# Optimization experiments

Hardware: AMD Instinct MI355X
Metric: run time of the kernel (lower is better)

The kernel has to match this reference:

```python
import jax, jax.numpy as jnp
import numpy as np

B, S, D, H, M, V, R = 2, 1024, 768, 8, 3072, 32000, 2
HD = D // H  # head_dim = qkv_dim // num_heads


def ln(x, scale, bias, eps=1e-6):
    m = jnp.mean(x, axis=-1, keepdims=True)
    v = jnp.mean(jnp.square(x - m), axis=-1, keepdims=True)
    return (x - m) * jax.lax.rsqrt(v + eps) * scale + bias


def setup_inputs() -> dict:
    key = jax.random.key(0)
    ks = jax.random.split(key, 16)
    r = lambda i, shp, s=0.02: jax.random.normal(ks[i], shp, jnp.float32) * s
    z = lambda shp: jnp.zeros(shp, jnp.float32)
    o = lambda shp: jnp.ones(shp, jnp.float32)
    return {
        'l2r_embed': jax.random.normal(ks[0], (B, S, D), jnp.float32),
        'r2l_embed': jax.random.normal(ks[1], (B, S, D), jnp.float32),
        'temb': jax.random.normal(ks[2], (B, D), jnp.float32),
        'ln_l2r_s': o((D,)), 'ln_l2r_b': z((D,)),
        'ln_r2l_s': o((D,)), 'ln_r2l_b': z((D,)),
        'Wq': r(3, (D, H, HD)), 'bq': z((H, HD)),
        'Wk': r(4, (D, H, HD)), 'bk': z((H, HD)),
        'Wv': r(5, (D, H, HD)), 'bv': z((H, HD)),
        'Wo': r(6, (H, HD, D)), 'bo': z((D,)),
        'ff_ln_s': o((D,)), 'ff_ln_b': z((D,)),
        'ff_w1': r(7, (D, M)), 'ff_b1': z((M,)),
        'ff_w2': r(8, (M, D)), 'ff_b2': z((D,)),
        'tm_w1': r(9, (D, M)), 'tm_b1': z((M,)),
        'tm_w2': r(10, (M, 4 * D)), 'tm_b2': z((4 * D,)),
        'film_w': r(11, (R, 4 * D, 2 * D)), 'film_b': z((R, 2 * D)),
        'r_w1': r(12, (R, D, M)), 'r_b1': z((R, M)),
        'r_w2': r(13, (R, M, D)), 'r_b2': z((R, D)),
        'r_ln_s': o((R, D)), 'r_ln_b': z((R, D)),
        'out_w': r(14, (D, V)), 'out_b': z((V,)),
    }


def reference(l2r_embed, r2l_embed, temb, ln_l2r_s, ln_l2r_b, ln_r2l_s, ln_r2l_b,
              Wq, bq, Wk, bk, Wv, bv, Wo, bo, ff_ln_s, ff_ln_b,
              ff_w1, ff_b1, ff_w2, ff_b2, tm_w1, tm_b1, tm_w2, tm_b2,
              film_w, film_b, r_w1, r_b1, r_w2, r_b2, r_ln_s, r_ln_b,
              out_w, out_b):
    inputs = l2r_embed + r2l_embed
    # prenorm on each direction (temb stays raw)
    l2r_n = ln(l2r_embed, ln_l2r_s, ln_l2r_b)
    r2l_n = ln(r2l_embed, ln_r2l_s, ln_r2l_b)
    # cross attention: query from sum, keys/vals from [temb, l2r, r2l]
    q = jnp.einsum('bsd,dhk->bshk', l2r_n + r2l_n, Wq) + bq
    all_e = jnp.concatenate([temb[:, None, :], l2r_n, r2l_n], axis=1)  # [B, 2S+1, D]
    k = jnp.einsum('bsd,dhk->bshk', all_e, Wk) + bk
    v = jnp.einsum('bsd,dhk->bshk', all_e, Wv) + bv
    q = q / jnp.sqrt(jnp.float32(HD))
    logits = jnp.einsum('bqhd,bkhd->bhqk', q, k)  # [B, H, S, 2S+1]
    idx = jnp.arange(S)
    l2r_mask = idx[:, None] >= idx[None, :]
    r2l_mask = idx[:, None] <= idx[None, :]
    joint = jnp.concatenate(
        [jnp.ones((S, 1), bool), l2r_mask, r2l_mask], axis=-1)[None, None]
    aw = jax.nn.softmax(
        jnp.where(joint, logits, jnp.finfo(jnp.float32).min), axis=-1)
    x = jnp.einsum('bhqk,bkhd->bqhd', aw, v)
    x = jnp.einsum('bqhd,hde->bqe', x, Wo) + bo
    x = x + inputs
    # prenorm FF block
    z = ln(x, ff_ln_s, ff_ln_b)
    z = jax.nn.relu(z @ ff_w1 + ff_b1) @ ff_w2 + ff_b2
    x = x + z
    # residual readout with FiLM conditioning
    t = jax.nn.gelu(temb @ tm_w1 + tm_b1) @ tm_w2 + tm_b2  # [B, 4D]
    for i in range(R):
        film = t @ film_w[i] + film_b[i]  # [B, 2D]
        z = jax.nn.gelu(x @ r_w1[i] + r_b1[i]) @ r_w2[i] + r_b2[i]
        x = ln(x + z, r_ln_s[i], r_ln_b[i])
        a, b = jnp.split(film[:, None, :], 2, axis=-1)
        x = a * x + b
    return x @ out_w + out_b  # [B, S, V]
```

## Files before the change

### kernel.cpp

```cpp
#include <hip/hip_runtime.h>
#include <cstdint>
#include <cstddef>

#define Bb 2
#define Ss 1024
#define Dd 768
#define Hh 8
#define HDh 96
#define Mm 3072
#define Vv 32000
#define KVr 2049

typedef __attribute__((ext_vector_type(8))) short short8v;
typedef __attribute__((ext_vector_type(4))) short short4v;
typedef __attribute__((ext_vector_type(4))) float f32x4;

#define GL16(gp, lp) __builtin_amdgcn_global_load_lds( \
    (const __attribute__((address_space(1))) void*)(gp), \
    (__attribute__((address_space(3))) void*)(lp), 16, 0, 0)

static __device__ __forceinline__ short f2bf(float f) {
  union { float f; unsigned u; } x; x.f = f;
  unsigned r = (x.u + 0x7FFFu + ((x.u >> 16) & 1u)) >> 16;
  return (short)(r & 0xFFFFu);
}

static __device__ __forceinline__ float gelu_f(float v) {
  float u = 0.7978845608028654f * (v + 0.044715f * v * v * v);
  float au = fabsf(u);
  float e = __expf(2.f * au);
  float t = 1.f - 2.f / (e + 1.f);
  return 0.5f * v * (1.f + copysignf(t, u));
}

static __device__ __forceinline__ float blk_sum(float val, float* sh) {
  #pragma unroll
  for (int off = 32; off >= 1; off >>= 1) val += __shfl_xor(val, off);
  __syncthreads();
  if ((threadIdx.x & 63) == 0) sh[threadIdx.x >> 6] = val;
  __syncthreads();
  return sh[0] + sh[1] + sh[2] + sh[3];
}

__global__ __launch_bounds__(256) void prep_kernel(
    const float* __restrict__ l2r, const float* __restrict__ r2l,
    const float* __restrict__ temb,
    const float* __restrict__ s1, const float* __restrict__ b1,
    const float* __restrict__ s2, const float* __restrict__ b2,
    float* __restrict__ inputs, short* __restrict__ qin, short* __restrict__ all_e)
{
  __shared__ float sh[4];
  const int tid = threadIdx.x;
  if (blockIdx.x >= 2048) {
    int b = blockIdx.x - 2048;
    #pragma unroll
    for (int i = 0; i < 3; ++i)
      all_e[(size_t)b * KVr * Dd + tid + i * 256] = f2bf(temb[(size_t)b * Dd + tid + i * 256]);
    return;
  }
  const int row = blockIdx.x;
  const int b = row >> 10, s = row & 1023;
  const float* ap = l2r + (size_t)row * Dd;
  const float* cp = r2l + (size_t)row * Dd;
  float a0 = ap[tid], a1 = ap[tid + 256], a2 = ap[tid + 512];
  float c0 = cp[tid], c1 = cp[tid + 256], c2 = cp[tid + 512];
  float ma = blk_sum(a0 + a1 + a2, sh) * (1.f / 768.f);
  float mc = blk_sum(c0 + c1 + c2, sh) * (1.f / 768.f);
  float va = blk_sum((a0-ma)*(a0-ma) + (a1-ma)*(a1-ma) + (a2-ma)*(a2-ma), sh) * (1.f / 768.f);
  float vc = blk_sum((c0-mc)*(c0-mc) + (c1-mc)*(c1-mc) + (c2-mc)*(c2-mc), sh) * (1.f / 768.f);
  float ia = rsqrtf(va + 1e-6f), ic = rsqrtf(vc + 1e-6f);
  size_t ro = (size_t)row * Dd;
  size_t e1 = ((size_t)b * KVr + 1 + s) * Dd;
  size_t e2 = ((size_t)b * KVr + 1 + Ss + s) * Dd;
  float av[3] = {a0, a1, a2}, cv[3] = {c0, c1, c2};
  #pragma unroll
  for (int i = 0; i < 3; ++i) {
    int c = tid + i * 256;
    float an = (av[i] - ma) * ia * s1[c] + b1[c];
    float cn = (cv[i] - mc) * ic * s2[c] + b2[c];
    inputs[ro + c] = av[i] + cv[i];
    qin[ro + c]    = f2bf(an + cn);
    all_e[e1 + c]  = f2bf(an);
    all_e[e2 + c]  = f2bf(cn);
  }
}

__global__ __launch_bounds__(256) void ln_comb2(
    const float* __restrict__ pk,
    const float* __restrict__ bias, const float* __restrict__ res,
    const float* __restrict__ sc, const float* __restrict__ bi,
    float* __restrict__ yf, short* __restrict__ yb)
{
  __shared__ float sh[4];
  const int row = blockIdx.x, tid = threadIdx.x;
  const size_t PS = (size_t)2048 * 768;
  size_t ro = (size_t)row * Dd;
  float vv[3];
  #pragma unroll
  for (int i = 0; i < 3; ++i) {
    int c = tid + i * 256;
    vv[i] = pk[ro + c] + pk[PS + ro + c] + bias[c] + res[ro + c];
  }
  float m = blk_sum(vv[0] + vv[1] + vv[2], sh) * (1.f / 768.f);
  float var = blk_sum((vv[0]-m)*(vv[0]-m) + (vv[1]-m)*(vv[1]-m) + (vv[2]-m)*(vv[2]-m), sh) * (1.f / 768.f);
  float inv = rsqrtf(var + 1e-6f);
  #pragma unroll
  for (int i = 0; i < 3; ++i) {
    int c = tid + i * 256;
    yf[ro + c] = vv[i];
    yb[ro + c] = f2bf((vv[i] - m) * inv * sc[c] + bi[c]);
  }
}

__global__ __launch_bounds__(256) void scale_comb(
    const float* __restrict__ pk, const float* __restrict__ bias,
    short* __restrict__ yb, float scale)
{
  const int row = blockIdx.x, tid = threadIdx.x;
  const size_t PS = (size_t)2048 * 768;
  size_t ro = (size_t)row * Dd;
  #pragma unroll
  for (int i = 0; i < 3; ++i) {
    int c = tid + i * 256;
    yb[ro + c] = f2bf((pk[ro + c] + pk[PS + ro + c] + bias[c]) * scale);
  }
}

__global__ __launch_bounds__(256) void ln_comb(
    const float* __restrict__ pk,
    const float* __restrict__ bias, const float* __restrict__ res,
    const float* __restrict__ sc, const float* __restrict__ bi,
    const float* __restrict__ film, float* __restrict__ yf, short* __restrict__ yb)
{
  __shared__ float sh[4];
  const int row = blockIdx.x, tid = threadIdx.x;
  const size_t PS = (size_t)2048 * 768;
  size_t ro = (size_t)row * Dd;
  float vv[3];
  #pragma unroll
  for (int i = 0; i < 3; ++i) {
    int c = tid + i * 256;
    float v = bias[c] + res[ro + c];
    #pragma unroll
    for (int s = 0; s < 4; ++s) v += pk[s * PS + ro + c];
    vv[i] = v;
  }
  float m = blk_sum(vv[0] + vv[1] + vv[2], sh) * (1.f / 768.f);
  float var = blk_sum((vv[0]-m)*(vv[0]-m) + (vv[1]-m)*(vv[1]-m) + (vv[2]-m)*(vv[2]-m), sh) * (1.f / 768.f);
  float inv = rsqrtf(var + 1e-6f);
  int bb = row >> 10;
  #pragma unroll
  for (int i = 0; i < 3; ++i) {
    int c = tid + i * 256;
    float o = (vv[i] - m) * inv * sc[c] + bi[c];
    o = film[(size_t)bb * 1536 + c] * o + film[(size_t)bb * 1536 + 768 + c];
    if (yf) yf[ro + c] = o;
    if (yb) yb[ro + c] = f2bf(o);
  }
}

__global__ __launch_bounds__(256) void combine_kernel(
    const float* __restrict__ pk,
    const float* __restrict__ bias, const float* __restrict__ res,
    float* __restrict__ yf, short* __restrict__ yb)
{
  const int row = blockIdx.x, tid = threadIdx.x;
  const size_t PS = (size_t)2048 * 768;
  size_t ro = (size_t)row * Dd;
  #pragma unroll
  for (int i = 0; i < 3; ++i) {
    int c = tid + i * 256;
    float v = bias[c] + res[ro + c];
    #pragma unroll
    for (int s = 0; s < 4; ++s) v += pk[s * PS + ro + c];
    yf[ro + c] = v;
    yb[ro + c] = f2bf(v);
  }
}

__global__ __launch_bounds__(256) void convT(const float* __restrict__ W, short* __restrict__ Wt,
                                             int K, int N, int ntile)
{
  __shared__ short T[64][72];
  const int bn = blockIdx.x % ntile, bk = blockIdx.x / ntile;
  const int k0 = bk * 64, n0 = bn * 64, tid = threadIdx.x;
  #pragma unroll
  for (int i = 0; i < 4; ++i) {
    int id = i * 256 + tid;
    int r = id >> 4, c4 = (id & 15) * 4;
    float4 w4 = *(const float4*)(W + (size_t)(k0 + r) * N + n0 + c4);
    T[c4 + 0][r] = f2bf(w4.x);
    T[c4 + 1][r] = f2bf(w4.y);
    T[c4 + 2][r] = f2bf(w4.z);
    T[c4 + 3][r] = f2bf(w4.w);
  }
  __syncthreads();
  #pragma unroll
  for (int i = 0; i < 4; ++i) {
    int id = i * 256 + tid;
    int n = id >> 4, k4 = (id & 15) * 4;
    short4v s = *(const short4v*)&T[n][k4];
    *(short4v*)(Wt + (size_t)(n0 + n) * K + k0 + k4) = s;
  }
}

__global__ __launch_bounds__(256) void convT2(const float* __restrict__ W1, short* __restrict__ D1,
                                              const float* __restrict__ W2, short* __restrict__ D2)
{
  __shared__ short T[64][72];
  const int tid = threadIdx.x;
  const bool second = blockIdx.x >= 576;
  const int id576 = second ? (blockIdx.x - 576) : blockIdx.x;
  const int K = second ? 3072 : 768;
  const int N = second ? 768 : 3072;
  const int ntile = N >> 6;
  const float* W = second ? W2 : W1;
  short* Wt = second ? D2 : D1;
  const int bn = id576 % ntile, bk = id576 / ntile;
  const int k0 = bk * 64, n0 = bn * 64;
  #pragma unroll
  for (int i = 0; i < 4; ++i) {
    int id = i * 256 + tid;
    int r = id >> 4, c4 = (id & 15) * 4;
    float4 w4 = *(const float4*)(W + (size_t)(k0 + r) * N + n0 + c4);
    T[c4 + 0][r] = f2bf(w4.x);
    T[c4 + 1][r] = f2bf(w4.y);
    T[c4 + 2][r] = f2bf(w4.z);
    T[c4 + 3][r] = f2bf(w4.w);
  }
  __syncthreads();
  #pragma unroll
  for (int i = 0; i < 4; ++i) {
    int id = i * 256 + tid;
    int n = id >> 4, k4 = (id & 15) * 4;
    short4v s = *(const short4v*)&T[n][k4];
    *(short4v*)(Wt + (size_t)(n0 + n) * K + k0 + k4) = s;
  }
}

__global__ __launch_bounds__(256) void convT4(const float* __restrict__ W0, const float* __restrict__ W1,
                                              const float* __restrict__ W2, const float* __restrict__ W3,
                                              const float* __restrict__ bk, const float* __restrict__ bv,
                                              short* __restrict__ Wt, float* __restrict__ kvb,
                                              const float* __restrict__ part2c, const float* __restrict__ fb,
                                              float* __restrict__ f0, float* __restrict__ f1)
{
  __shared__ short T[64][72];
  const int tid = threadIdx.x;
  if (blockIdx.x >= 577) {
    const int n = (blockIdx.x - 577) * 256 + tid;
    float a0 = fb[n], a1 = a0;
    for (int s = 0; s < 64; ++s) {
      a0 += part2c[(size_t)s * 6144 + n];
      a1 += part2c[(size_t)s * 6144 + 3072 + n];
    }
    float* dst = (n < 1536) ? f0 : f1;
    const int c = (n >= 1536) ? (n - 1536) : n;
    dst[c] = a0;
    dst[1536 + c] = a1;
    return;
  }
  if (blockIdx.x == 576) {
    #pragma unroll
    for (int i = 0; i < 6; ++i) {
      int c = i * 256 + tid;
      if (c < 1536) kvb[c] = (c < 768) ? bk[c] : bv[c - 768];
    }
    return;
  }
  const int wsel = blockIdx.x / 144, rem = blockIdx.x % 144;
  const float* W = wsel == 0 ? W0 : wsel == 1 ? W1 : wsel == 2 ? W2 : W3;
  short* dst = Wt + (size_t)wsel * 768 * 768;
  const int bn = rem % 12, bk2 = rem / 12;
  const int k0 = bk2 * 64, n0 = bn * 64;
  #pragma unroll
  for (int i = 0; i < 4; ++i) {
    int id = i * 256 + tid;
    int r = id >> 4, c4 = (id & 15) * 4;
    float4 w4 = *(const float4*)(W + (size_t)(k0 + r) * 768 + n0 + c4);
    T[c4 + 0][r] = f2bf(w4.x);
    T[c4 + 1][r] = f2bf(w4.y);
    T[c4 + 2][r] = f2bf(w4.z);
    T[c4 + 3][r] = f2bf(w4.w);
  }
  __syncthreads();
  #pragma unroll
  for (int i = 0; i < 4; ++i) {
    int id = i * 256 + tid;
    int n = id >> 4, k4 = (id & 15) * 4;
    short4v s = *(const short4v*)&T[n][k4];
    *(short4v*)(dst + (size_t)(n0 + n) * 768 + k0 + k4) = s;
  }
}

template<int ACT>
__global__ __launch_bounds__(256, 4) void gemm_bf(
    const short* __restrict__ A, const short* __restrict__ Bt,
    const float* __restrict__ bias, const float* __restrict__ res,
    float* __restrict__ C, short* __restrict__ Cbf, float* __restrict__ Cpart,
    int M, int N, int K, float scale, int mtiles, int ntiles, int ksplit)
{
  __shared__ short As[2][4096];
  __shared__ short Bs[2][4096];
  const int tid = threadIdx.x, lane = tid & 63, wv = tid >> 6;
  const int l15 = lane & 15, l4 = lane >> 4;

  const int nwg = gridDim.x;
  const int qc = nwg >> 3, rc = nwg & 7;
  const int xcd = blockIdx.x & 7, idx = blockIdx.x >> 3;
  const int wgid = (xcd < rc ? xcd * (qc + 1) : rc * (qc + 1) + (xcd - rc) * qc) + idx;
  const int by = wgid % mtiles;
  const int rest = wgid / mtiles;
  const int bx = rest % ntiles;
  const int sp = rest / ntiles;
  const int kper = K / ksplit;
  const int kbeg = sp * kper;
  const int NT = kper >> 5;

  const int m0 = by * 128, n0 = bx * 128;
  const int wm = (wv >> 1) * 64, wn = (wv & 1) * 64;

  const int srow = lane >> 2, schunk = lane & 3;
  const int scsw = (schunk ^ ((srow >> 1) & 3)) << 3;
  const short* sA = A + (size_t)(m0 + wv * 32 + srow) * K + kbeg + scsw;
  const short* sB = Bt + (size_t)(n0 + wv * 32 + srow) * K + kbeg + scsw;
  const int stBase = wv * 1024;
  const int frsw = (l4 ^ ((l15 >> 1) & 3)) << 3;

  f32x4 acc[4][4];
  const f32x4 zz = {0.f, 0.f, 0.f, 0.f};
  #pragma unroll
  for (int i = 0; i < 4; ++i)
    #pragma unroll
    for (int j = 0; j < 4; ++j) acc[i][j] = zz;

  GL16(sA, &As[0][stBase]);
  GL16(sA + (size_t)16 * K, &As[0][stBase + 512]);
  GL16(sB, &Bs[0][stBase]);
  GL16(sB + (size_t)16 * K, &Bs[0][stBase + 512]);

  int buf = 0;
  for (int t = 0; t < NT; ++t) {
    if (t + 1 < NT) {
      int k0 = (t + 1) << 5;
      GL16(sA + k0, &As[buf ^ 1][stBase]);
      GL16(sA + (size_t)16 * K + k0, &As[buf ^ 1][stBase + 512]);
      GL16(sB + k0, &Bs[buf ^ 1][stBase]);
      GL16(sB + (size_t)16 * K + k0, &Bs[buf ^ 1][stBase + 512]);
      asm volatile("s_waitcnt vmcnt(4)" ::: "memory");
    } else {
      asm volatile("s_waitcnt vmcnt(0)" ::: "memory");
    }
    __builtin_amdgcn_s_barrier();

    short8v af[4], bfv[4];
    #pragma unroll
    for (int mi = 0; mi < 4; ++mi)
      af[mi] = *(const short8v*)&As[buf][(wm + mi * 16 + l15) * 32 + frsw];
    #pragma unroll
    for (int ni = 0; ni < 4; ++ni)
      bfv[ni] = *(const short8v*)&Bs[buf][(wn + ni * 16 + l15) * 32 + frsw];
    __builtin_amdgcn_s_setprio(1);
    #pragma unroll
    for (int mi = 0; mi < 4; ++mi)
      #pragma unroll
      for (int ni = 0; ni < 4; ++ni)
        acc[mi][ni] = __builtin_amdgcn_mfma_f32_16x16x32_bf16(af[mi], bfv[ni], acc[mi][ni], 0, 0, 0);
    __builtin_amdgcn_s_setprio(0);
    if (t + 1 < NT) __builtin_amdgcn_s_barrier();
    buf ^= 1;
  }

  if (Cpart) {
    float* Cp = Cpart + (size_t)sp * M * N;
    #pragma unroll
    for (int mi = 0; mi < 4; ++mi)
      #pragma unroll
      for (int r = 0; r < 4; ++r) {
        int row = m0 + wm + mi * 16 + l4 * 4 + r;
        if (row >= M) continue;
        size_t rb = (size_t)row * N;
        #pragma unroll
        for (int ni = 0; ni < 4; ++ni)
          Cp[rb + n0 + wn + ni * 16 + l15] = acc[mi][ni][r];
      }
    return;
  }

  #pragma unroll
  for (int mi = 0; mi < 4; ++mi) {
    #pragma unroll
    for (int r = 0; r < 4; ++r) {
      int row = m0 + wm + mi * 16 + l4 * 4 + r;
      if (row >= M) continue;
      size_t rb = (size_t)row * N;
      #pragma unroll
      for (int ni = 0; ni < 4; ++ni) {
        int col = n0 + wn + ni * 16 + l15;
        float val = (acc[mi][ni][r] + bias[col]) * scale;
        if (ACT == 1) val = fmaxf(val, 0.f);
        if (ACT == 2) val = gelu_f(val);
        if (res) val += res[rb + col];
        if (C)   C[rb + col] = val;
        if (Cbf) Cbf[rb + col] = f2bf(val);
      }
    }
  }
}

__global__ __launch_bounds__(512, 2) void gemm256(
    const short* __restrict__ A, const short* __restrict__ Bt,
    const float* __restrict__ bias, float* __restrict__ C,
    int M, int N, int K, int mtiles)
{
  __shared__ short As[2][16384];
  __shared__ short Bs[2][16384];
  const int tid = threadIdx.x, lane = tid & 63, wv = tid >> 6;
  const int l15 = lane & 15, l4 = lane >> 4;

  const int nwg = gridDim.x;
  const int qc = nwg >> 3, rc = nwg & 7;
  const int xcd = blockIdx.x & 7, idx = blockIdx.x >> 3;
  const int wgid = (xcd < rc ? xcd * (qc + 1) : rc * (qc + 1) + (xcd - rc) * qc) + idx;
  const int by = wgid % mtiles, bx = wgid / mtiles;
  const int m0 = by * 256, n0 = bx * 256;
  const int wm = (wv >> 2) * 128, wn = (wv & 3) * 64;

  const int srow = lane >> 2, schunk = lane & 3;
  const int scsw = (schunk ^ ((srow >> 1) & 3)) << 3;
  const short* sA = A + (size_t)(m0 + wv * 16 + srow) * K + scsw;
  const short* sB = Bt + (size_t)(n0 + wv * 16 + srow) * K + scsw;
  const int stBase = wv * 512;
  const int frsw = (l4 ^ ((l15 >> 1) & 3)) << 3;

  #define STG_A(b, kk, ko) do { \
    GL16(sA + (ko) + (kk) * 32,                  &As[b][(kk) * 8192 + stBase]); \
    GL16(sA + (size_t)128 * K + (ko) + (kk) * 32, &As[b][(kk) * 8192 + 4096 + stBase]); } while (0)
  #define STG_B(b, kk, ko) do { \
    GL16(sB + (ko) + (kk) * 32,                  &Bs[b][(kk) * 8192 + stBase]); \
    GL16(sB + (size_t)128 * K + (ko) + (kk) * 32, &Bs[b][(kk) * 8192 + 4096 + stBase]); } while (0)
  #define ARD(b, kk, row) (*(const short8v*)&As[b][(kk) * 8192 + (row) * 32 + frsw])
  #define BRD(b, kk, row) (*(const short8v*)&Bs[b][(kk) * 8192 + (row) * 32 + frsw])

  f32x4 acc[8][4];
  const f32x4 zz = {0.f, 0.f, 0.f, 0.f};
  #pragma unroll
  for (int i = 0; i < 8; ++i)
    #pragma unroll
    for (int j = 0; j < 4; ++j) acc[i][j] = zz;

  const int NT = K >> 6;

  STG_A(0, 0, 0); STG_B(0, 0, 0); STG_A(0, 1, 0); STG_B(0, 1, 0);
  asm volatile("s_waitcnt vmcnt(4)" ::: "memory");
  __builtin_amdgcn_s_barrier();

  int buf = 0;
  for (int t = 0; t < NT; ++t) {
    const bool pf = (t + 1 < NT);
    const int k1 = (t + 1) << 6;
    short8v af[4], bfv[4];

    #pragma unroll
    for (int mi = 0; mi < 4; ++mi) af[mi] = ARD(buf, 0, wm + mi * 16 + l15);
    #pragma unroll
    for (int ni = 0; ni < 4; ++ni) bfv[ni] = BRD(buf, 0, wn + ni * 16 + l15);
    if (pf) STG_A(buf ^ 1, 0, k1);
    __builtin_amdgcn_s_barrier();
    asm volatile("s_waitcnt lgkmcnt(0)" ::: "memory");
    __builtin_amdgcn_sched_barrier(0);
    __builtin_amdgcn_s_setprio(1);
    #pragma unroll
    for (int mi = 0; mi < 4; ++mi)
      #pragma unroll
      for (int ni = 0; ni < 4; ++ni)
        acc[mi][ni] = __builtin_amdgcn_mfma_f32_16x16x32_bf16(af[mi], bfv[ni], acc[mi][ni], 0, 0, 0);
    __builtin_amdgcn_s_setprio(0);
    __builtin_amdgcn_s_barrier();

    #pragma unroll
    for (int mi = 0; mi < 4; ++mi) af[mi] = ARD(buf, 0, wm + 64 + mi * 16 + l15);
    if (pf) STG_B(buf ^ 1, 0, k1);
    __builtin_amdgcn_s_barrier();
    asm volatile("s_waitcnt lgkmcnt(0)" ::: "memory");
    __builtin_amdgcn_sched_barrier(0);
    __builtin_amdgcn_s_setprio(1);
    #pragma unroll
    for (int mi = 0; mi < 4; ++mi)
      #pragma unroll
      for (int ni = 0; ni < 4; ++ni)
        acc[4 + mi][ni] = __builtin_amdgcn_mfma_f32_16x16x32_bf16(af[mi], bfv[ni], acc[4 + mi][ni], 0, 0, 0);
    __builtin_amdgcn_s_setprio(0);
    if (pf) asm volatile("s_waitcnt vmcnt(4)" ::: "memory");
    else    asm volatile("s_waitcnt vmcnt(0)" ::: "memory");
    __builtin_amdgcn_s_barrier();

    #pragma unroll
    for (int mi = 0; mi < 4; ++mi) af[mi] = ARD(buf, 1, wm + mi * 16 + l15);
    #pragma unroll
    for (int ni = 0; ni < 4; ++ni) bfv[ni] = BRD(buf, 1, wn + ni * 16 + l15);
    if (pf) STG_A(buf ^ 1, 1, k1);
    __builtin_amdgcn_s_barrier();
    asm volatile("s_waitcnt lgkmcnt(0)" ::: "memory");
    __builtin_amdgcn_sched_barrier(0);
    __builtin_amdgcn_s_setprio(1);
    #pragma unroll
    for (int mi = 0; mi < 4; ++mi)
      #pragma unroll
      for (int ni = 0; ni < 4; ++ni)
        acc[mi][ni] = __builtin_amdgcn_mfma_f32_16x16x32_bf16(af[mi], bfv[ni], acc[mi][ni], 0, 0, 0);
    __builtin_amdgcn_s_setprio(0);
    __builtin_amdgcn_s_barrier();

    #pragma unroll
    for (int mi = 0; mi < 4; ++mi) af[mi] = ARD(buf, 1, wm + 64 + mi * 16 + l15);
    if (pf) STG_B(buf ^ 1, 1, k1);
    __builtin_amdgcn_s_barrier();
    asm volatile("s_waitcnt lgkmcnt(0)" ::: "memory");
    __builtin_amdgcn_sched_barrier(0);
    __builtin_amdgcn_s_setprio(1);
    #pragma unroll
    for (int mi = 0; mi < 4; ++mi)
      #pragma unroll
      for (int ni = 0; ni < 4; ++ni)
        acc[4 + mi][ni] = __builtin_amdgcn_mfma_f32_16x16x32_bf16(af[mi], bfv[ni], acc[4 + mi][ni], 0, 0, 0);
    __builtin_amdgcn_s_setprio(0);
    if (pf) asm volatile("s_waitcnt vmcnt(4)" ::: "memory");
    __builtin_amdgcn_s_barrier();

    buf ^= 1;
  }

  #pragma unroll
  for (int mi = 0; mi < 8; ++mi) {
    #pragma unroll
    for (int r = 0; r < 4; ++r) {
      int row = m0 + wm + mi * 16 + l4 * 4 + r;
      size_t rb = (size_t)row * N;
      #pragma unroll
      for (int ni = 0; ni < 4; ++ni) {
        int col = n0 + wn + ni * 16 + l15;
        C[rb + col] = acc[mi][ni][r] + bias[col];
      }
    }
  }
  #undef STG_A
  #undef STG_B
  #undef ARD
  #undef BRD
}

__global__ __launch_bounds__(256) void attn_kernel(
    const short* __restrict__ q, const short* __restrict__ kv,
    float* __restrict__ Op0, float* __restrict__ Op1, float* __restrict__ ml)
{
  __shared__ short Kls[64][104];
  __shared__ short Vt[96][72];
  __shared__ short Pls[4][16][72];

  const int tid = threadIdx.x, lane = tid & 63, w = tid >> 6;
  const int l15 = lane & 15, l4 = lane >> 4;
  const int chunk = blockIdx.x >> 8;
  const int inner = blockIdx.x & 255;
  const int qt = inner & 15;
  const int bh = inner >> 4;
  const int h = bh & 7, b = bh >> 3;
  const int qb = qt * 64;
  const int qw = qb + w * 16;

  short8v qf[3];
  {
    const short* qp = q + ((size_t)(b * Ss + qw + l15)) * Dd + h * HDh + l4 * 8;
    #pragma unroll
    for (int kk = 0; kk < 3; ++kk) qf[kk] = *(const short8v*)(qp + kk * 32);
  }

  const f32x4 zz = {0.f, 0.f, 0.f, 0.f};
  f32x4 Oa[6];
  #pragma unroll
  for (int fn = 0; fn < 6; ++fn) Oa[fn] = zz;
  float mrow[4], lrow[4];
  #pragma unroll
  for (int r = 0; r < 4; ++r) { mrow[r] = -3.0e38f; lrow[r] = 0.f; }

  const size_t kvbase = (size_t)b * KVr;

  for (int t = chunk; t < 33; t += 2) {
    int k0 = t * 64;
    bool l2r_vis = (k0 <= Ss) && (k0 - 1 <= qb + 63);
    int rmaxk = (k0 + 63 > 2 * Ss) ? 2 * Ss : (k0 + 63);
    bool r2l_vis = (k0 + 63 >= Ss + 1) && (rmaxk - (Ss + 1) >= qb);
    if (!(t == 0 || l2r_vis || r2l_vis)) continue;

    __syncthreads();
    #pragma unroll
    for (int i = 0; i < 3; ++i) {
      int id = i * 256 + tid;
      int row = id / 12, cc = (id % 12) * 8;
      const short* kp = kv + (kvbase + k0 + row) * 1536 + h * HDh + cc;
      short8v k8 = *(const short8v*)kp;
      *(short8v*)&Kls[row][cc] = k8;
      short8v v8 = *(const short8v*)(kp + 768);
      #pragma unroll
      for (int j = 0; j < 8; ++j) Vt[cc + j][row] = v8[j];
    }
    __syncthreads();

    f32x4 sc[4];
    #pragma unroll
    for (int nt = 0; nt < 4; ++nt) {
      f32x4 d = zz;
      #pragma unroll
      for (int kk = 0; kk < 3; ++kk) {
        short8v kf = *(const short8v*)&Kls[nt * 16 + l15][kk * 32 + l4 * 8];
        d = __builtin_amdgcn_mfma_f32_16x16x32_bf16(qf[kk], kf, d, 0, 0, 0);
      }
      sc[nt] = d;
    }
    float tmax[4] = {-3.0e38f, -3.0e38f, -3.0e38f, -3.0e38f};
    #pragma unroll
    for (int nt = 0; nt < 4; ++nt)
      #pragma unroll
      for (int r = 0; r < 4; ++r) {
        int qg = qw + l4 * 4 + r;
        int j = k0 + nt * 16 + l15;
        bool vis = (j == 0) ||
                   (j >= 1 && j <= Ss && (j - 1) <= qg) ||
                   (j >= Ss + 1 && j <= 2 * Ss && (j - (Ss + 1)) >= qg);
        if (!vis) sc[nt][r] = -3.0e38f;
        tmax[r] = fmaxf(tmax[r], sc[nt][r]);
      }
    #pragma unroll
    for (int r = 0; r < 4; ++r) {
      #pragma unroll
      for (int off = 8; off >= 1; off >>= 1) tmax[r] = fmaxf(tmax[r], __shfl_xor(tmax[r], off));
    }
    float scl[4];
    #pragma unroll
    for (int r = 0; r < 4; ++r) {
      float mnew = fmaxf(mrow[r], tmax[r]);
      scl[r] = __expf(mrow[r] - mnew);
      mrow[r] = mnew;
    }
    #pragma unroll
    for (int fn = 0; fn < 6; ++fn)
      #pragma unroll
      for (int r = 0; r < 4; ++r) Oa[fn][r] *= scl[r];
    float lad[4] = {0.f, 0.f, 0.f, 0.f};
    #pragma unroll
    for (int nt = 0; nt < 4; ++nt)
      #pragma unroll
      for (int r = 0; r < 4; ++r) {
        float p = __expf(sc[nt][r] - mrow[r]);
        lad[r] += p;
        Pls[w][l4 * 4 + r][nt * 16 + l15] = f2bf(p);
      }
    #pragma unroll
    for (int r = 0; r < 4; ++r) {
      #pragma unroll
      for (int off = 8; off >= 1; off >>= 1) lad[r] += __shfl_xor(lad[r], off);
      lrow[r] = lrow[r] * scl[r] + lad[r];
    }
    __syncthreads();

    short8v pf[2];
    #pragma unroll
    for (int kk = 0; kk < 2; ++kk) pf[kk] = *(const short8v*)&Pls[w][l15][kk * 32 + l4 * 8];
    #pragma unroll
    for (int fn = 0; fn < 6; ++fn) {
      #pragma unroll
      for (int kk = 0; kk < 2; ++kk) {
        short8v vf = *(const short8v*)&Vt[fn * 16 + l15][kk * 32 + l4 * 8];
        Oa[fn] = __builtin_amdgcn_mfma_f32_16x16x32_bf16(pf[kk], vf, Oa[fn], 0, 0, 0);
      }
    }
  }

  float* Op = chunk ? Op1 : Op0;
  #pragma unroll
  for (int fn = 0; fn < 6; ++fn)
    #pragma unroll
    for (int r = 0; r < 4; ++r) {
      int row = qw + l4 * 4 + r;
      int col = h * HDh + fn * 16 + l15;
      Op[((size_t)(b * Ss + row)) * Dd + col] = Oa[fn][r];
    }
  if (l15 == 0) {
    #pragma unroll
    for (int r = 0; r < 4; ++r) {
      int row = qw + l4 * 4 + r;
      size_t ix = ((size_t)((chunk * 2 + b) * 8 + h) * 1024 + row) * 2;
      ml[ix] = mrow[r];
      ml[ix + 1] = lrow[r];
    }
  }
}

__global__ __launch_bounds__(256) void attn_merge(
    const float* __restrict__ Op0, const float* __restrict__ Op1,
    const float* __restrict__ ml, short* __restrict__ o)
{
  const int row = blockIdx.x, tid = threadIdx.x;
  const int b = row >> 10, s = row & 1023;
  size_t ro = (size_t)row * Dd;
  #pragma unroll
  for (int i = 0; i < 3; ++i) {
    int c = tid + i * 256;
    int h = c / HDh;
    size_t ix = ((size_t)(b * 8 + h) * 1024 + s) * 2;
    float m0 = ml[ix],         l0 = ml[ix + 1];
    float m1 = ml[32768 + ix], l1 = ml[32768 + ix + 1];
    float mm = fmaxf(m0, m1);
    float s0 = __expf(m0 - mm), s1 = __expf(m1 - mm);
    float denom = s0 * l0 + s1 * l1;
    o[ro + c] = f2bf((s0 * Op0[ro + c] + s1 * Op1[ro + c]) / denom);
  }
}

__global__ __launch_bounds__(256) void thin1(const float* __restrict__ A, const float* __restrict__ W,
                                             float* __restrict__ part, int K, int N, int nblk, int splits)
{
  __shared__ float a0s[64], a1s[64];
  const int nb = blockIdx.x % nblk, ks = blockIdx.x / nblk;
  const int kl = K / splits, kbeg = ks * kl;
  const int tid = threadIdx.x;
  for (int k = tid; k < kl; k += 256) { a0s[k] = A[kbeg + k]; a1s[k] = A[K + kbeg + k]; }
  __syncthreads();
  const int n = nb * 256 + tid;
  float acc0 = 0.f, acc1 = 0.f;
  for (int k = 0; k < kl; ++k) {
    float w = W[(size_t)(kbeg + k) * N + n];
    acc0 = fmaf(a0s[k], w, acc0);
    acc1 = fmaf(a1s[k], w, acc1);
  }
  part[(size_t)ks * 2 * N + n] = acc0;
  part[(size_t)ks * 2 * N + N + n] = acc1;
}

__global__ __launch_bounds__(256) void thin1p(
    const float* __restrict__ pin, const float* __restrict__ bin,
    const float* __restrict__ W, float* __restrict__ part)
{
  __shared__ float a0s[48], a1s[48];
  const int nb = blockIdx.x % 12, ks = blockIdx.x / 12;
  const int kbeg = ks * 48, tid = threadIdx.x;
  for (int j = tid; j < 96; j += 256) {
    int row = j / 48, k = j % 48;
    float v = bin[kbeg + k];
    for (int s = 0; s < 64; ++s) v += pin[(size_t)s * 6144 + (size_t)row * 3072 + kbeg + k];
    v = gelu_f(v);
    if (row) a1s[k] = v; else a0s[k] = v;
  }
  __syncthreads();
  const int n = nb * 256 + tid;
  float acc0 = 0.f, acc1 = 0.f;
  for (int k = 0; k < 48; ++k) {
    float w = W[(size_t)(kbeg + k) * 3072 + n];
    acc0 = fmaf(a0s[k], w, acc0);
    acc1 = fmaf(a1s[k], w, acc1);
  }
  part[(size_t)ks * 6144 + n] = acc0;
  part[(size_t)ks * 6144 + 3072 + n] = acc1;
}

__global__ __launch_bounds__(256) void film1p(
    const float* __restrict__ pin, const float* __restrict__ bin,
    const float* __restrict__ W, float* __restrict__ part)
{
  __shared__ float a0s[48], a1s[48];
  const int nb = blockIdx.x % 12, ks = blockIdx.x / 12;
  const int kbeg = ks * 48, tid = threadIdx.x;
  for (int j = tid; j < 96; j += 256) {
    int row = j / 48, k = j % 48;
    float v = bin[kbeg + k];
    for (int s = 0; s < 64; ++s) v += pin[(size_t)s * 6144 + (size_t)row * 3072 + kbeg + k];
    if (row) a1s[k] = v; else a0s[k] = v;
  }
  __syncthreads();
  const int n = nb * 256 + tid;
  const int col = (n >= 1536) ? (n - 1536) : n;
  const float* Wp = W + ((n < 1536) ? (size_t)0 : (size_t)3072 * 1536)
                      + (size_t)kbeg * 1536 + col;
  float acc0 = 0.f, acc1 = 0.f;
  for (int k = 0; k < 48; ++k) {
    float w = Wp[(size_t)k * 1536];
    acc0 = fmaf(a0s[k], w, acc0);
    acc1 = fmaf(a1s[k], w, acc1);
  }
  part[(size_t)ks * 6144 + n] = acc0;
  part[(size_t)ks * 6144 + 3072 + n] = acc1;
}

static void gemm_launch(int act, const short* A, const short* Bt, const float* bias,
                        const float* res, float* C, short* Cbf, float* Cpart,
                        int M, int N, int K, float scale, int ksplit, hipStream_t s)
{
  int mt = (M + 127) >> 7, nt = N >> 7;
  dim3 grid(mt * nt * ksplit), blk(256);
  if (act == 1)      gemm_bf<1><<<grid, blk, 0, s>>>(A, Bt, bias, res, C, Cbf, Cpart, M, N, K, scale, mt, nt, ksplit);
  else if (act == 2) gemm_bf<2><<<grid, blk, 0, s>>>(A, Bt, bias, res, C, Cbf, Cpart, M, N, K, scale, mt, nt, ksplit);
  else               gemm_bf<0><<<grid, blk, 0, s>>>(A, Bt, bias, res, C, Cbf, Cpart, M, N, K, scale, mt, nt, ksplit);
}

static void conv_launch(const float* W, short* Wt, int K, int N, hipStream_t s)
{
  int nt = N >> 6, kt = K >> 6;
  convT<<<dim3(nt * kt), dim3(256), 0, s>>>(W, Wt, K, N, nt);
}

extern "C" void kernel_launch(void* const* d_in, const int* in_sizes, int n_in,
                              void* d_out, int out_size, void* d_ws, size_t ws_size,
                              hipStream_t stream)
{
  (void)in_sizes; (void)n_in; (void)out_size; (void)ws_size;
  const float* l2r      = (const float*)d_in[0];
  const float* r2l      = (const float*)d_in[1];
  const float* temb     = (const float*)d_in[2];
  const float* ln_l2r_s = (const float*)d_in[3];
  const float* ln_l2r_b = (const float*)d_in[4];
  const float* ln_r2l_s = (const float*)d_in[5];
  const float* ln_r2l_b = (const float*)d_in[6];
  const float* Wq = (const float*)d_in[7];
  const float* bq = (const float*)d_in[8];
  const float* Wk = (const float*)d_in[9];
  const float* bk = (const float*)d_in[10];
  const float* Wv = (const float*)d_in[11];
  const float* bv = (const float*)d_in[12];
  const float* Wo = (const float*)d_in[13];
  const float* bo = (const float*)d_in[14];
  const float* ff_ln_s = (const float*)d_in[15];
  const float* ff_ln_b = (const float*)d_in[16];
  const float* ff_w1 = (const float*)d_in[17];
  const float* ff_b1 = (const float*)d_in[18];
  const float* ff_w2 = (const float*)d_in[19];
  const float* ff_b2 = (const float*)d_in[20];
  const float* tm_w1 = (const float*)d_in[21];
  const float* tm_b1 = (const float*)d_in[22];
  const float* tm_w2 = (const float*)d_in[23];
  const float* tm_b2 = (const float*)d_in[24];
  const float* film_w = (const float*)d_in[25];
  const float* film_b = (const float*)d_in[26];
  const float* r_w1 = (const float*)d_in[27];
  const float* r_b1 = (const float*)d_in[28];
  const float* r_w2 = (const float*)d_in[29];
  const float* r_b2 = (const float*)d_in[30];
  const float* r_ln_s = (const float*)d_in[31];
  const float* r_ln_b = (const float*)d_in[32];
  const float* out_w = (const float*)d_in[33];
  const float* out_b = (const float*)d_in[34];

  uint8_t* base = (uint8_t*)d_ws;
  short* qin_bf  = (short*)(base + 0);
  short* alle_bf = (short*)(base + 3145728);
  short* qb      = (short*)(base + 9440256);
  short* kvbuf   = (short*)(base + 12585984);
  short* attn_bf = (short*)(base + 25175040);
  float* inputs  = (float*)(base + 28320768);
  float* xbuf    = (float*)(base + 34612224);
  short* xn_bf   = (short*)(base + 40903680);
  short* big_bf  = (short*)(base + 44049408);
  float* x2f     = (float*)(base + 56632320);
  short* x2bf    = (short*)(base + 62923776);
  float* x3f     = (float*)(base + 72360960);
  short* x3bf    = (short*)(base + 78652416);
  short* x4bf    = (short*)(base + 81798144);
  short* wslot   = (short*)(base + 84943872);
  uint8_t* sm    = base + 89662464;
  float* f0    = (float*)(sm + 0);
  float* f1    = (float*)(sm + 12288);
  float* kvbia = (float*)(sm + 24576);
  short* w2slot = (short*)inputs;
  float* part2a = (float*)(base + 44049408);
  float* part2b = (float*)(base + 44049408 + 1572864);
  float* part2c = (float*)(base + 44049408 + 3145728);
  float* qpart = (float*)(base + 56632320);
  float* Op0 = (float*)(base + 0);
  float* mlb = (float*)(base + 6291456);
  float* Op1 = xbuf;
  float* wopart = (float*)(base + 0);
  float* partK = (float*)(base + 0);
  short* outwT = (short*)(base + 0);

  const float qscale = 0.1020620726159658f;
  dim3 blk(256);

  thin1<<<dim3(12 * 64), blk, 0, stream>>>(temb, tm_w1, part2a, 768, 3072, 12, 64);
  thin1p<<<dim3(12 * 64), blk, 0, stream>>>(part2a, tm_b1, tm_w2, part2b);
  film1p<<<dim3(12 * 64), blk, 0, stream>>>(part2b, tm_b2, film_w, part2c);

  prep_kernel<<<2050, blk, 0, stream>>>(l2r, r2l, temb, ln_l2r_s, ln_l2r_b, ln_r2l_s, ln_r2l_b,
                                        inputs, qin_bf, alle_bf);

  convT4<<<dim3(589), blk, 0, stream>>>(Wq, Wk, Wv, Wo, bk, bv, wslot, kvbia,
                                        part2c, film_b, f0, f1);

  gemm_launch(0, qin_bf, wslot, bq, nullptr, nullptr, nullptr, qpart, 2048, 768, 768, 1.f, 2, stream);
  scale_comb<<<2048, blk, 0, stream>>>(qpart, bq, qb, qscale);
  gemm_launch(0, alle_bf, wslot + (size_t)768 * 768, kvbia, nullptr, nullptr, kvbuf, nullptr, 4098, 1536, 768, 1.f, 1, stream);

  attn_kernel<<<512, blk, 0, stream>>>(qb, kvbuf, Op0, Op1, mlb);
  attn_merge<<<2048, blk, 0, stream>>>(Op0, Op1, mlb, attn_bf);

  gemm_launch(0, attn_bf, wslot + (size_t)3 * 768 * 768, bo, nullptr, nullptr, nullptr, wopart, 2048, 768, 768, 1.f, 2, stream);
  ln_comb2<<<2048, blk, 0, stream>>>(wopart, bo, inputs, ff_ln_s, ff_ln_b, xbuf, xn_bf);

  convT2<<<dim3(1152), blk, 0, stream>>>(ff_w1, wslot, ff_w2, w2slot);
  gemm_launch(1, xn_bf, wslot, ff_b1, nullptr, nullptr, big_bf, nullptr, 2048, 3072, 768, 1.f, 1, stream);
  gemm_launch(0, big_bf, w2slot, nullptr, nullptr, nullptr, nullptr, partK, 2048, 768, 3072, 1.f, 4, stream);
  combine_kernel<<<2048, blk, 0, stream>>>(partK, ff_b2, xbuf, x2f, x2bf);

  convT2<<<dim3(1152), blk, 0, stream>>>(r_w1, wslot, r_w2, w2slot);
  gemm_launch(2, x2bf, wslot, r_b1, nullptr, nullptr, big_bf, nullptr, 2048, 3072, 768, 1.f, 1, stream);
  gemm_launch(0, big_bf, w2slot, nullptr, nullptr, nullptr, nullptr, partK, 2048, 768, 3072, 1.f, 4, stream);
  ln_comb<<<2048, blk, 0, stream>>>(partK, r_b2, x2f, r_ln_s, r_ln_b, f0, x3f, x3bf);

  convT2<<<dim3(1152), blk, 0, stream>>>(r_w1 + (size_t)768 * 3072, wslot,
                                         r_w2 + (size_t)3072 * 768, w2slot);
  gemm_launch(2, x3bf, wslot, r_b1 + 3072, nullptr, nullptr, big_bf, nullptr, 2048, 3072, 768, 1.f, 1, stream);
  gemm_launch(0, big_bf, w2slot, nullptr, nullptr, nullptr, nullptr, partK, 2048, 768, 3072, 1.f, 4, stream);
  ln_comb<<<2048, blk, 0, stream>>>(partK, r_b2 + 768, x3f, r_ln_s + 768, r_ln_b + 768, f1, nullptr, x4bf);

  conv_launch(out_w, outwT, 768, 32000, stream);
  gemm256<<<dim3(8 * 125), dim3(512), 0, stream>>>(x4bf, outwT, out_b, (float*)d_out,
                                                   2048, 32000, 768, 8);
}
```

Before: 542.2 us.

## Fold Q projection into KV GEMM via linearity and split attention into four chunks

Uses linearity, Wq(l2r_n + r2l_n) = Wq l2r_n + Wq r2l_n, to compute Q projections inside the combined K/V GEMM over all_e (N widened from 1536 to 2304). A small kernel then sums the two bf16 per-direction Q rows, adds the bias and scales. This drops a separate split-K GEMM and its combine pass. Attention key tiles are split four ways instead of two (1024 blocks), and the merge now combines four partial softmax states. The cost is more partial-output traffic, a slightly larger KV GEMM, and extra rounding because Q is summed after a bf16 round.

Result: no change. 544.3 us (+0.4%).

```diff
diff --git a/kernel.cpp b/kernel.cpp
--- a/kernel.cpp
+++ b/kernel.cpp
@@ -25,6 +25,11 @@
   return (short)(r & 0xFFFFu);
 }
 
+static __device__ __forceinline__ float bf2f(short s) {
+  union { unsigned u; float f; } x; x.u = ((unsigned)(unsigned short)s) << 16;
+  return x.f;
+}
+
 static __device__ __forceinline__ float gelu_f(float v) {
   float u = 0.7978845608028654f * (v + 0.044715f * v * v * v);
   float au = fabsf(u);
@@ -47,7 +52,7 @@
     const float* __restrict__ temb,
     const float* __restrict__ s1, const float* __restrict__ b1,
     const float* __restrict__ s2, const float* __restrict__ b2,
-    float* __restrict__ inputs, short* __restrict__ qin, short* __restrict__ all_e)
+    float* __restrict__ inputs, short* __restrict__ all_e)
 {
   __shared__ float sh[4];
   const int tid = threadIdx.x;
@@ -79,9 +84,23 @@
     float an = (av[i] - ma) * ia * s1[c] + b1[c];
     float cn = (cv[i] - mc) * ic * s2[c] + b2[c];
     inputs[ro + c] = av[i] + cv[i];
-    qin[ro + c]    = f2bf(an + cn);
     all_e[e1 + c]  = f2bf(an);
     all_e[e2 + c]  = f2bf(cn);
+  }
+}
+
+__global__ __launch_bounds__(256) void qsum_kernel(
+    const short* __restrict__ kvq, const float* __restrict__ bq,
+    short* __restrict__ qb, float scale)
+{
+  const int row = blockIdx.x, tid = threadIdx.x;
+  const int b = row >> 10, s = row & 1023;
+  const short* p1 = kvq + ((size_t)b * KVr + 1 + s) * 2304;
+  const short* p2 = kvq + ((size_t)b * KVr + 1 + Ss + s) * 2304;
+  #pragma unroll
+  for (int i = 0; i < 3; ++i) {
+    int c = tid + i * 256;
+    qb[(size_t)row * Dd + c] = f2bf((bf2f(p1[c]) + bf2f(p2[c]) + bq[c]) * scale);
   }
 }
 
@@ -109,20 +128,6 @@
     int c = tid + i * 256;
     yf[ro + c] = vv[i];
     yb[ro + c] = f2bf((vv[i] - m) * inv * sc[c] + bi[c]);
-  }
-}
-
-__global__ __launch_bounds__(256) void scale_comb(
-    const float* __restrict__ pk, const float* __restrict__ bias,
-    short* __restrict__ yb, float scale)
-{
-  const int row = blockIdx.x, tid = threadIdx.x;
-  const size_t PS = (size_t)2048 * 768;
-  size_t ro = (size_t)row * Dd;
-  #pragma unroll
-  for (int i = 0; i < 3; ++i) {
-    int c = tid + i * 256;
-    yb[ro + c] = f2bf((pk[ro + c] + pk[PS + ro + c] + bias[c]) * scale);
   }
 }
 
@@ -262,9 +267,9 @@
   }
   if (blockIdx.x == 576) {
     #pragma unroll
-    for (int i = 0; i < 6; ++i) {
+    for (int i = 0; i < 9; ++i) {
       int c = i * 256 + tid;
-      if (c < 1536) kvb[c] = (c < 768) ? bk[c] : bv[c - 768];
+      if (c < 2304) kvb[c] = (c < 768) ? 0.f : (c < 1536 ? bk[c - 768] : bv[c - 1536]);
     }
     return;
   }
@@ -551,8 +556,9 @@
 }
 
 __global__ __launch_bounds__(256) void attn_kernel(
-    const short* __restrict__ q, const short* __restrict__ kv,
-    float* __restrict__ Op0, float* __restrict__ Op1, float* __restrict__ ml)
+    const short* __restrict__ q, const short* __restrict__ kvq,
+    float* __restrict__ Op0, float* __restrict__ Op1,
+    float* __restrict__ Op2, float* __restrict__ Op3, float* __restrict__ ml)
 {
   __shared__ short Kls[64][104];
   __shared__ short Vt[96][72];
@@ -585,7 +591,7 @@
 
   const size_t kvbase = (size_t)b * KVr;
 
-  for (int t = chunk; t < 33; t += 2) {
+  for (int t = chunk; t < 33; t += 4) {
     int k0 = t * 64;
     bool l2r_vis = (k0 <= Ss) && (k0 - 1 <= qb + 63);
     int rmaxk = (k0 + 63 > 2 * Ss) ? 2 * Ss : (k0 + 63);
@@ -597,7 +603,9 @@
     for (int i = 0; i < 3; ++i) {
       int id = i * 256 + tid;
       int row = id / 12, cc = (id % 12) * 8;
-      const short* kp = kv + (kvbase + k0 + row) * 1536 + h * HDh + cc;
+      int key = k0 + row;
+      if (key > 2 * Ss) key = 2 * Ss;
+      const short* kp = kvq + (kvbase + key) * 2304 + 768 + h * HDh + cc;
       short8v k8 = *(const short8v*)kp;
       *(short8v*)&Kls[row][cc] = k8;
       short8v v8 = *(const short8v*)(kp + 768);
@@ -676,7 +684,7 @@
     }
   }
 
-  float* Op = chunk ? Op1 : Op0;
+  float* Op = (chunk == 0) ? Op0 : (chunk == 1) ? Op1 : (chunk == 2) ? Op2 : Op3;
   #pragma unroll
   for (int fn = 0; fn < 6; ++fn)
     #pragma unroll
@@ -689,7 +697,7 @@
     #pragma unroll
     for (int r = 0; r < 4; ++r) {
       int row = qw + l4 * 4 + r;
-      size_t ix = ((size_t)((chunk * 2 + b) * 8 + h) * 1024 + row) * 2;
+      size_t ix = (size_t)chunk * 32768 + (((size_t)(b * 8 + h) * 1024 + row) * 2);
       ml[ix] = mrow[r];
       ml[ix + 1] = lrow[r];
     }
@@ -698,6 +706,7 @@
 
 __global__ __launch_bounds__(256) void attn_merge(
     const float* __restrict__ Op0, const float* __restrict__ Op1,
+    const float* __restrict__ Op2, const float* __restrict__ Op3,
     const float* __restrict__ ml, short* __restrict__ o)
 {
   const int row = blockIdx.x, tid = threadIdx.x;
@@ -708,12 +717,16 @@
     int c = tid + i * 256;
     int h = c / HDh;
     size_t ix = ((size_t)(b * 8 + h) * 1024 + s) * 2;
-    float m0 = ml[ix],         l0 = ml[ix + 1];
+    float m0 = ml[ix], l0 = ml[ix + 1];
     float m1 = ml[32768 + ix], l1 = ml[32768 + ix + 1];
-    float mm = fmaxf(m0, m1);
+    float m2 = ml[65536 + ix], l2 = ml[65536 + ix + 1];
+    float m3 = ml[98304 + ix], l3 = ml[98304 + ix + 1];
+    float mm = fmaxf(fmaxf(m0, m1), fmaxf(m2, m3));
     float s0 = __expf(m0 - mm), s1 = __expf(m1 - mm);
-    float denom = s0 * l0 + s1 * l1;
-    o[ro + c] = f2bf((s0 * Op0[ro + c] + s1 * Op1[ro + c]) / denom);
+    float s2 = __expf(m2 - mm), s3 = __expf(m3 - mm);
+    float denom = s0 * l0 + s1 * l1 + s2 * l2 + s3 * l3;
+    float val = s0 * Op0[ro + c] + s1 * Op1[ro + c] + s2 * Op2[ro + c] + s3 * Op3[ro + c];
+    o[ro + c] = f2bf(val / denom);
   }
 }
 
@@ -850,34 +863,34 @@
   const float* out_b = (const float*)d_in[34];
 
   uint8_t* base = (uint8_t*)d_ws;
-  short* qin_bf  = (short*)(base + 0);
+  short* qb      = (short*)(base + 0);
   short* alle_bf = (short*)(base + 3145728);
-  short* qb      = (short*)(base + 9440256);
-  short* kvbuf   = (short*)(base + 12585984);
-  short* attn_bf = (short*)(base + 25175040);
-  float* inputs  = (float*)(base + 28320768);
-  float* xbuf    = (float*)(base + 34612224);
-  short* xn_bf   = (short*)(base + 40903680);
-  short* big_bf  = (short*)(base + 44049408);
-  float* x2f     = (float*)(base + 56632320);
-  short* x2bf    = (short*)(base + 62923776);
-  float* x3f     = (float*)(base + 72360960);
-  short* x3bf    = (short*)(base + 78652416);
-  short* x4bf    = (short*)(base + 81798144);
-  short* wslot   = (short*)(base + 84943872);
-  uint8_t* sm    = base + 89662464;
+  short* kvq     = (short*)(base + 9440256);
+  short* attn_bf = (short*)(base + 12585984);
+  float* inputs  = (float*)(base + 28323840);
+  float* xbuf    = (float*)(base + 34615296);
+  short* xn_bf   = (short*)(base + 40906752);
+  short* big_bf  = (short*)(base + 44052480);
+  float* x2f     = (float*)(base + 56635392);
+  short* x2bf    = (short*)(base + 62926848);
+  float* x3f     = (float*)(base + 66072576);
+  short* x3bf    = (short*)(base + 72364032);
+  short* x4bf    = (short*)(base + 75509760);
+  short* wslot   = (short*)(base + 78655488);
+  uint8_t* sm    = base + 83374080;
   float* f0    = (float*)(sm + 0);
   float* f1    = (float*)(sm + 12288);
   float* kvbia = (float*)(sm + 24576);
   short* w2slot = (short*)inputs;
-  float* part2a = (float*)(base + 44049408);
-  float* part2b = (float*)(base + 44049408 + 1572864);
-  float* part2c = (float*)(base + 44049408 + 3145728);
-  float* qpart = (float*)(base + 56632320);
-  float* Op0 = (float*)(base + 0);
-  float* mlb = (float*)(base + 6291456);
+  float* part2a = (float*)(base + 44052480);
+  float* part2b = (float*)(base + 44052480 + 1572864);
+  float* part2c = (float*)(base + 44052480 + 3145728);
+  float* Op0 = (float*)(base + 3145728);
   float* Op1 = xbuf;
-  float* wopart = (float*)(base + 0);
+  float* Op2 = (float*)(base + 44052480);
+  float* Op3 = (float*)(base + 50343936);
+  float* mlb = (float*)(base + 56635392);
+  float* wopart = (float*)(base + 44052480);
   float* partK = (float*)(base + 0);
   short* outwT = (short*)(base + 0);
 
@@ -889,17 +902,16 @@
   film1p<<<dim3(12 * 64), blk, 0, stream>>>(part2b, tm_b2, film_w, part2c);
 
   prep_kernel<<<2050, blk, 0, stream>>>(l2r, r2l, temb, ln_l2r_s, ln_l2r_b, ln_r2l_s, ln_r2l_b,
-                                        inputs, qin_bf, alle_bf);
+                                        inputs, alle_bf);
 
   convT4<<<dim3(589), blk, 0, stream>>>(Wq, Wk, Wv, Wo, bk, bv, wslot, kvbia,
                                         part2c, film_b, f0, f1);
 
-  gemm_launch(0, qin_bf, wslot, bq, nullptr, nullptr, nullptr, qpart, 2048, 768, 768, 1.f, 2, stream);
-  scale_comb<<<2048, blk, 0, stream>>>(qpart, bq, qb, qscale);
-  gemm_launch(0, alle_bf, wslot + (size_t)768 * 768, kvbia, nullptr, nullptr, kvbuf, nullptr, 4098, 1536, 768, 1.f, 1, stream);
-
-  attn_kernel<<<512, blk, 0, stream>>>(qb, kvbuf, Op0, Op1, mlb);
-  attn_merge<<<2048, blk, 0, stream>>>(Op0, Op1, mlb, attn_bf);
+  gemm_launch(0, alle_bf, wslot, kvbia, nullptr, nullptr, kvq, nullptr, 4098, 2304, 768, 1.f, 1, stream);
+  qsum_kernel<<<2048, blk, 0, stream>>>(kvq, bq, qb, qscale);
+
+  attn_kernel<<<1024, blk, 0, stream>>>(qb, kvq, Op0, Op1, Op2, Op3, mlb);
+  attn_merge<<<2048, blk, 0, stream>>>(Op0, Op1, Op2, Op3, mlb, attn_bf);
 
   gemm_launch(0, attn_bf, wslot + (size_t)3 * 768 * 768, bo, nullptr, nullptr, nullptr, wopart, 2048, 768, 768, 1.f, 2, stream);
   ln_comb2<<<2048, blk, 0, stream>>>(wopart, bo, inputs, ff_ln_s, ff_ln_b, xbuf, xn_bf);
```
